# Kernel optimization log

Hardware: AMD Instinct MI355X
Metric: run time of the kernel (lower is better)

The kernel has to match this reference:

```python
import jax, jax.numpy as jnp
import numpy as np
from jax import lax

EPS = 1e-5
IC = 32  # inter_channels

def bn(x, g, b, m, v):
    sh = (1, -1, 1, 1)
    return (x - m.reshape(sh)) * (g.reshape(sh) * lax.rsqrt(v.reshape(sh) + EPS)) + b.reshape(sh)

def prelu(x, a):
    return jnp.where(x >= 0, x, a * x)

def conv1x1(x, w):  # x: [B,C,H,W], w: [O,C]
    return jnp.einsum('bchw,oc->bohw', x, w)

def dconv(x, w, d):  # 3x3 dilated conv, same padding
    return lax.conv_general_dilated(x, w, (1, 1), [(d, d), (d, d)], rhs_dilation=(d, d),
                                    dimension_numbers=('NCHW', 'OIHW', 'NCHW'))

def glca_forward(feature, q_w, q_gamma, q_beta, q_mean, q_var, q_alpha,
                 k_w, k_gamma, k_beta, k_mean, k_var, k_alpha,
                 v_w, v_gamma, v_beta, v_mean, v_var, v_alpha,
                 d1_w, d1_gamma, d1_beta, d1_mean, d1_var,
                 d2_w, d2_gamma, d2_beta, d2_mean, d2_var,
                 d3_w, d3_gamma, d3_beta, d3_mean, d3_var,
                 o_w, o_gamma, o_beta, o_mean, o_var, o_alpha):
    B, C, H, W = feature.shape
    q = prelu(bn(conv1x1(feature, q_w), q_gamma, q_beta, q_mean, q_var), q_alpha)  # [B,IC,H,W]
    k = prelu(bn(conv1x1(feature, k_w), k_gamma, k_beta, k_mean, k_var), k_alpha)
    val = prelu(bn(conv1x1(feature, v_w), v_gamma, v_beta, v_mean, v_var), v_alpha)
    qr = q.transpose(0, 3, 2, 1).reshape(B * W, H, IC)   # [BW,H,IC]
    kr = k.transpose(0, 3, 1, 2).reshape(B * W, IC, H)   # [BW,IC,H]
    att = jax.nn.softmax(jnp.matmul(qr, kr), axis=-1)    # [BW,H,H]
    branches = []
    for w, g, b, m, var, d in ((d1_w, d1_gamma, d1_beta, d1_mean, d1_var, 1),
                               (d2_w, d2_gamma, d2_beta, d2_mean, d2_var, 3),
                               (d3_w, d3_gamma, d3_beta, d3_mean, d3_var, 5)):
        t = jax.nn.relu(bn(dconv(val, w, d), g, b, m, var))          # [B,IC,H,W]
        # faithful to source: permute(0,3,1,2) then raw view to [BW,H,IC]
        t = t.transpose(0, 3, 1, 2).reshape(B * W, H, IC)
        branches.append(jnp.matmul(att, t))                          # [BW,H,IC]
    # faithful to source: cat along dim 0, then raw view(B,W,H,-1)
    res = jnp.concatenate(branches, axis=0).reshape(B, W, H, 3 * IC)
    res = res.transpose(0, 3, 2, 1)                                  # [B,3*IC,H,W]
    out = prelu(bn(conv1x1(res, o_w), o_gamma, o_beta, o_mean, o_var) + feature, o_alpha)
    return out

def setup_inputs() -> dict:
    B, C, H, W = 8, 256, 160, 160
    key = jax.random.key(0)
    ks = iter(jax.random.split(key, 48))
    d = {}
    d['feature'] = jax.random.normal(next(ks), (B, C, H, W), jnp.float32)
    for p in ('q', 'k', 'v'):
        d[p + '_w'] = jax.random.normal(next(ks), (IC, C), jnp.float32) * 0.05
        d[p + '_gamma'] = jax.random.uniform(next(ks), (IC,), jnp.float32, 0.5, 1.5)
        d[p + '_beta'] = jax.random.normal(next(ks), (IC,), jnp.float32) * 0.1
        d[p + '_mean'] = jax.random.normal(next(ks), (IC,), jnp.float32) * 0.1
        d[p + '_var'] = jax.random.uniform(next(ks), (IC,), jnp.float32, 0.5, 1.5)
        d[p + '_alpha'] = jnp.full((1,), 0.25, jnp.float32)
    for p in ('d1', 'd2', 'd3'):
        d[p + '_w'] = jax.random.normal(next(ks), (IC, IC, 3, 3), jnp.float32) * 0.05
        d[p + '_gamma'] = jax.random.uniform(next(ks), (IC,), jnp.float32, 0.5, 1.5)
        d[p + '_beta'] = jax.random.normal(next(ks), (IC,), jnp.float32) * 0.1
        d[p + '_mean'] = jax.random.normal(next(ks), (IC,), jnp.float32) * 0.1
        d[p + '_var'] = jax.random.uniform(next(ks), (IC,), jnp.float32, 0.5, 1.5)
    d['o_w'] = jax.random.normal(next(ks), (C, 3 * IC), jnp.float32) * 0.05
    d['o_gamma'] = jax.random.uniform(next(ks), (C,), jnp.float32, 0.5, 1.5)
    d['o_beta'] = jax.random.normal(next(ks), (C,), jnp.float32) * 0.1
    d['o_mean'] = jax.random.normal(next(ks), (C,), jnp.float32) * 0.1
    d['o_var'] = jax.random.uniform(next(ks), (C,), jnp.float32, 0.5, 1.5)
    d['o_alpha'] = jnp.full((1,), 0.25, jnp.float32)
    return d

def reference(feature, q_w, q_gamma, q_beta, q_mean, q_var, q_alpha,
              k_w, k_gamma, k_beta, k_mean, k_var, k_alpha,
              v_w, v_gamma, v_beta, v_mean, v_var, v_alpha,
              d1_w, d1_gamma, d1_beta, d1_mean, d1_var,
              d2_w, d2_gamma, d2_beta, d2_mean, d2_var,
              d3_w, d3_gamma, d3_beta, d3_mean, d3_var,
              o_w, o_gamma, o_beta, o_mean, o_var, o_alpha):
    return glca_forward(feature, q_w, q_gamma, q_beta, q_mean, q_var, q_alpha,
                        k_w, k_gamma, k_beta, k_mean, k_var, k_alpha,
                        v_w, v_gamma, v_beta, v_mean, v_var, v_alpha,
                        d1_w, d1_gamma, d1_beta, d1_mean, d1_var,
                        d2_w, d2_gamma, d2_beta, d2_mean, d2_var,
                        d3_w, d3_gamma, d3_beta, d3_mean, d3_var,
                        o_w, o_gamma, o_beta, o_mean, o_var, o_alpha)
```

## Files before the change

kernel.cpp:

```cpp
#include <hip/hip_runtime.h>

constexpr int Hh = 160, Ww = 160, Bb = 8, Cc = 256, ICn = 32;
constexpr int HWn = Hh * Ww;
constexpr float EPSf = 1e-5f;

constexpr int P_WQH  = 0;
constexpr int P_WQL  = 12288;
constexpr int P_QKVB = 24576;
constexpr int P_QKVA = 24672;
constexpr int P_DWB  = 24768;
constexpr int P_DB   = 52416;
constexpr int P_OWB  = 52512;
constexpr int P_OB   = 77088;
constexpr int P_OA   = 77344;
constexpr int PLANE  = Bb * ICn * HWn;
constexpr int OFF_Q  = 77824;
constexpr int OFF_K  = OFF_Q + PLANE;
constexpr int OFF_V  = OFF_Q + 2 * PLANE;
constexpr int OFF_T  = OFF_Q + 3 * PLANE;
constexpr int OFF_TPF= OFF_T + (3 * PLANE) / 2;
constexpr int OFF_CAT= OFF_Q + 6 * PLANE;

typedef unsigned short u16;
typedef short bf16x8 __attribute__((ext_vector_type(8)));
typedef float f32x4  __attribute__((ext_vector_type(4)));

__device__ __forceinline__ unsigned f2b(float x) {
    unsigned u = __float_as_uint(x);
    return (u + 0x7FFFu + ((u >> 16) & 1u)) >> 16;
}
__device__ __forceinline__ float b2f(unsigned b) { return __uint_as_float(b << 16); }

struct InPtrs { const float* p[40]; };

__global__ void k_prep(InPtrs in, float* __restrict__ ws) {
    int idx = blockIdx.x * 256 + threadIdx.x;
    if (idx < 24576) {
        int oc = idx >> 8, c = idx & 255;
        int z = oc >> 5, o = oc & 31;
        const float* wz = in.p[1 + 6 * z];
        float s = in.p[2 + 6 * z][o] * rsqrtf(in.p[5 + 6 * z][o] + EPSf);
        float wf = wz[o * 256 + c] * s;
        unsigned hi = f2b(wf);
        unsigned lo = f2b(wf - b2f(hi));
        ((u16*)(ws + P_WQH))[oc * 256 + c] = (u16)hi;
        ((u16*)(ws + P_WQL))[oc * 256 + c] = (u16)lo;
    } else if (idx < 24672) {
        int oc = idx - 24576; int z = oc >> 5, o = oc & 31;
        float s = in.p[2 + 6 * z][o] * rsqrtf(in.p[5 + 6 * z][o] + EPSf);
        ws[P_QKVB + oc] = in.p[3 + 6 * z][o] - in.p[4 + 6 * z][o] * s;
    } else if (idx < 24768) {
        int oc = idx - 24672; int z = oc >> 5;
        ws[P_QKVA + oc] = in.p[6 + 6 * z][0];
    } else if (idx < 52416) {
        int j = idx - 24768;
        int d = j / 9216, r2 = j % 9216;
        int oc = r2 & 31; int tmp = r2 >> 5;
        int kx = tmp % 3; tmp /= 3; int ky = tmp % 3; int ic2 = tmp / 3;
        const float* wd = in.p[19 + 5 * d];
        float s = in.p[20 + 5 * d][oc] * rsqrtf(in.p[23 + 5 * d][oc] + EPSf);
        float wf = wd[((oc * 32 + ic2) * 3 + ky) * 3 + kx] * s;
        ((u16*)(ws + P_DWB))[((d * 9 + ky * 3 + kx) * 32 + oc) * 32 + ic2] = (u16)f2b(wf);
    } else if (idx < 52512) {
        int j = idx - 52416; int d = j >> 5, oc = j & 31;
        float s = in.p[20 + 5 * d][oc] * rsqrtf(in.p[23 + 5 * d][oc] + EPSf);
        ws[P_DB + j] = in.p[21 + 5 * d][oc] - in.p[22 + 5 * d][oc] * s;
    } else if (idx < 77088) {
        int j2 = idx - 52512; int c = j2 / 96;
        float s = in.p[35][c] * rsqrtf(in.p[38][c] + EPSf);
        ((u16*)(ws + P_OWB))[j2] = (u16)f2b(in.p[34][j2] * s);
    } else if (idx < 77344) {
        int c = idx - 77088;
        float s = in.p[35][c] * rsqrtf(in.p[38][c] + EPSf);
        ws[P_OB + c] = in.p[36][c] - in.p[37][c] * s;
    } else if (idx == 77344) {
        ws[P_OA] = in.p[39][0];
    }
}

__global__ __launch_bounds__(64) void k_vpad(float* __restrict__ ws) {
    u16* Vt = (u16*)(ws + OFF_V);
    size_t base = (size_t)blockIdx.x * 176 * 32;
    int t = threadIdx.x;
    int off = (t < 32) ? t * 8 : (168 * 32 + (t - 32) * 8);
    uint4 z = {0u, 0u, 0u, 0u};
    *(uint4*)(Vt + base + off) = z;
}

__global__ __launch_bounds__(256) void k_qkv(const float* __restrict__ feat,
                                             float* __restrict__ ws) {
    __shared__ u16 BhS[8192];
    __shared__ u16 BlS[8192];
    const int tid = threadIdx.x;
    const int wv = tid >> 6, l = tid & 63;
    const int g = l >> 4, c15 = l & 15;
    const int n0 = blockIdx.x * 128;
    const int b = n0 / HWn, hw0 = n0 % HWn;
    const float* fbase = feat + (size_t)b * Cc * HWn + hw0;
    const u16* __restrict__ WQH = (const u16*)(ws + P_WQH);
    const u16* __restrict__ WQL = (const u16*)(ws + P_WQL);
    f32x4 acc[6][2];
    f32x4 z4 = {0.f, 0.f, 0.f, 0.f};
#pragma unroll
    for (int mt = 0; mt < 6; mt++) { acc[mt][0] = z4; acc[mt][1] = z4; }

    for (int kc = 0; kc < 4; kc++) {
        __syncthreads();
#pragma unroll
        for (int ss = 0; ss < 4; ss++) {
            int s = tid + ss * 256;
            int sl = s & 63, si = s >> 6;
            int k0 = kc * 64 + (si >> 3) * 32 + (sl >> 4) * 8;
            int nn = (si & 7) * 16 + (sl & 15);
            const float* gp = fbase + (size_t)k0 * HWn + nn;
            unsigned hb[8], lb[8];
#pragma unroll
            for (int v = 0; v < 8; v++) {
                float x = gp[(size_t)v * HWn];
                hb[v] = f2b(x);
                lb[v] = f2b(x - b2f(hb[v]));
            }
            uint4 hv = {hb[0] | (hb[1] << 16), hb[2] | (hb[3] << 16),
                        hb[4] | (hb[5] << 16), hb[6] | (hb[7] << 16)};
            uint4 lv = {lb[0] | (lb[1] << 16), lb[2] | (lb[3] << 16),
                        lb[4] | (lb[5] << 16), lb[6] | (lb[7] << 16)};
            *(uint4*)(&BhS[(si * 64 + sl) * 8]) = hv;
            *(uint4*)(&BlS[(si * 64 + sl) * 8]) = lv;
        }
        __syncthreads();
#pragma unroll
        for (int ks = 0; ks < 2; ks++) {
            bf16x8 bh[2], bl[2];
#pragma unroll
            for (int ntl = 0; ntl < 2; ntl++) {
                int nt = wv * 2 + ntl;
                bh[ntl] = *(const bf16x8*)(&BhS[((ks * 8 + nt) * 64 + l) * 8]);
                bl[ntl] = *(const bf16x8*)(&BlS[((ks * 8 + nt) * 64 + l) * 8]);
            }
#pragma unroll
            for (int mt = 0; mt < 6; mt++) {
                int arow = (16 * mt + c15) * 256 + kc * 64 + ks * 32 + g * 8;
                bf16x8 ah = *(const bf16x8*)(WQH + arow);
                bf16x8 al = *(const bf16x8*)(WQL + arow);
#pragma unroll
                for (int ntl = 0; ntl < 2; ntl++) {
                    acc[mt][ntl] = __builtin_amdgcn_mfma_f32_16x16x32_bf16(ah, bh[ntl], acc[mt][ntl], 0, 0, 0);
                    acc[mt][ntl] = __builtin_amdgcn_mfma_f32_16x16x32_bf16(ah, bl[ntl], acc[mt][ntl], 0, 0, 0);
                    acc[mt][ntl] = __builtin_amdgcn_mfma_f32_16x16x32_bf16(al, bh[ntl], acc[mt][ntl], 0, 0, 0);
                }
            }
        }
    }
    u16* vt = (u16*)(ws + OFF_V);
#pragma unroll
    for (int mt = 0; mt < 6; mt++)
#pragma unroll
        for (int ntl = 0; ntl < 2; ntl++) {
            int pos = hw0 + (wv * 2 + ntl) * 16 + c15;
            if (mt < 4) {
#pragma unroll
                for (int jr = 0; jr < 4; jr++) {
                    int oc = 16 * mt + 4 * g + jr;
                    float bb = ws[P_QKVB + oc];
                    float aa = ws[P_QKVA + oc];
                    float y = acc[mt][ntl][jr] + bb;
                    y = y >= 0.f ? y : aa * y;
                    int z = oc >> 5, o = oc & 31;
                    ws[OFF_Q + (size_t)z * PLANE + ((size_t)b * ICn + o) * HWn + pos] = y;
                }
            } else {
                int h = pos / 160, w2 = pos % 160;
                unsigned r[2];
#pragma unroll
                for (int p = 0; p < 2; p++) {
                    int oc = 16 * mt + 4 * g + 2 * p;
                    float y0 = acc[mt][ntl][2 * p]     + ws[P_QKVB + oc];
                    float y1 = acc[mt][ntl][2 * p + 1] + ws[P_QKVB + oc + 1];
                    float a0 = ws[P_QKVA + oc], a1 = ws[P_QKVA + oc + 1];
                    y0 = y0 >= 0.f ? y0 : a0 * y0;
                    y1 = y1 >= 0.f ? y1 : a1 * y1;
                    r[p] = f2b(y0) | (f2b(y1) << 16);
                }
                size_t a = ((size_t)(b * 160 + h) * 176 + w2 + 8) * 32 + (mt - 4) * 16 + 4 * g;
                uint2 dd; dd.x = r[0]; dd.y = r[1];
                *(uint2*)(vt + a) = dd;
            }
        }
}

__global__ __launch_bounds__(256) void k_dconv(float* __restrict__ ws) {
    const int tid = threadIdx.x;
    const int wv = tid >> 6, l = tid & 63;
    const int g = l >> 4, c15 = l & 15;
    const int b = blockIdx.y;
    const int d = blockIdx.z;
    const int dil = 1 + 2 * d;
    const int h0 = blockIdx.x * 2;
    const u16* __restrict__ WB = (const u16*)(ws + P_DWB) + d * 9 * 32 * 32;
    bf16x8 wb[9][2];
#pragma unroll
    for (int tap = 0; tap < 9; tap++)
#pragma unroll
        for (int n = 0; n < 2; n++)
            wb[tap][n] = *(const bf16x8*)(WB + ((size_t)tap * 32 + n * 16 + c15) * 32 + g * 8);
    const u16* __restrict__ Vt = (const u16*)(ws + OFF_V) + (size_t)b * 160 * 176 * 32;
    const float bias0 = ws[P_DB + d * 32 + c15];
    const float bias1 = ws[P_DB + d * 32 + 16 + c15];
    u16* __restrict__ tp = (u16*)(ws + OFF_TPF) + (size_t)(d * Bb + b) * ICn * HWn;
    f32x4 z4 = {0.f, 0.f, 0.f, 0.f};

    for (int t5 = 0; t5 < 5; t5++) {
        int t = wv * 5 + t5;
        int h = h0 + (t >= 10);
        int w0 = (t % 10) * 16;
        f32x4 acc0 = z4, acc1 = z4;
#pragma unroll
        for (int ky = 0; ky < 3; ky++) {
            int hh = h + dil * (ky - 1);
            if ((unsigned)hh >= 160u) continue;
            const u16* row = Vt + (size_t)hh * 176 * 32;
#pragma unroll
            for (int kx = 0; kx < 3; kx++) {
                int wbase = w0 + dil * (kx - 1) + 8;
                bf16x8 av = *(const bf16x8*)(row + (size_t)(wbase + c15) * 32 + g * 8);
                acc0 = __builtin_amdgcn_mfma_f32_16x16x32_bf16(av, wb[ky * 3 + kx][0], acc0, 0, 0, 0);
                acc1 = __builtin_amdgcn_mfma_f32_16x16x32_bf16(av, wb[ky * 3 + kx][1], acc1, 0, 0, 0);
            }
        }
        size_t pixb = (size_t)h * 160 + w0 + 4 * g;
        uint2 o0, o1;
        o0.x = f2b(fmaxf(acc0[0] + bias0, 0.f)) | (f2b(fmaxf(acc0[1] + bias0, 0.f)) << 16);
        o0.y = f2b(fmaxf(acc0[2] + bias0, 0.f)) | (f2b(fmaxf(acc0[3] + bias0, 0.f)) << 16);
        o1.x = f2b(fmaxf(acc1[0] + bias1, 0.f)) | (f2b(fmaxf(acc1[1] + bias1, 0.f)) << 16);
        o1.y = f2b(fmaxf(acc1[2] + bias1, 0.f)) | (f2b(fmaxf(acc1[3] + bias1, 0.f)) << 16);
        *(uint2*)(tp + (size_t)c15 * HWn + pixb) = o0;
        *(uint2*)(tp + (size_t)(16 + c15) * HWn + pixb) = o1;
    }
}

__global__ __launch_bounds__(256) void k_tfrag(float* __restrict__ ws) {
    __shared__ u16 fr[4][5120];
    const int tid = threadIdx.x;
    const int wq = blockIdx.x;
    const int b  = blockIdx.y;
    const int d  = blockIdx.z;
    const int w0 = wq * 4;
    const u16* __restrict__ tp = (const u16*)(ws + OFF_TPF) + (size_t)(d * Bb + b) * ICn * HWn;
    for (int i = tid; i < 5120; i += 256) {
        int ic = i / 160, h = i % 160;
        uint2 v = *(const uint2*)(tp + (size_t)ic * HWn + h * Ww + w0);
        fr[0][i] = (u16)(v.x & 0xFFFFu);
        fr[1][i] = (u16)(v.x >> 16);
        fr[2][i] = (u16)(v.y & 0xFFFFu);
        fr[3][i] = (u16)(v.y >> 16);
    }
    __syncthreads();
    u16* __restrict__ tf = (u16*)(ws + OFF_T);
#pragma unroll
    for (int it = 0; it < 10; it++) {
        int W = tid + it * 256;
        int s = W / 640, word = W % 640;
        int slot = word >> 6, lane = word & 63;
        int jc = (lane & 15) | ((slot / 5) << 4);
        int h2b = ((slot % 5) << 5) | (((lane >> 4) & 3) << 3);
        unsigned r[4];
#pragma unroll
        for (int p = 0; p < 4; p++) {
            int f0 = (h2b + 2 * p) * 32 + jc;
            unsigned lo = fr[s][f0];
            unsigned hi = fr[s][f0 + 32];
            r[p] = lo | (hi << 16);
        }
        uint4 o4 = {r[0], r[1], r[2], r[3]};
        *(uint4*)(tf + ((size_t)d * 1280 + b * 160 + w0 + s) * 5120 + word * 8) = o4;
    }
}

__device__ __forceinline__ void stage_qk_hilo(const float* __restrict__ g,
                                              char* hi_buf, char* lo_buf, int tid) {
#pragma unroll
    for (int ss = 0; ss < 2; ss++) {
        int s = tid + ss * 320;
        int l = s & 63, rt = s >> 6;
        int h = 16 * rt + (l & 15);
        int icb = (l >> 4) * 8;
        const float* gp = g + (size_t)icb * HWn + h * Ww;
        unsigned hb[8], lb[8];
#pragma unroll
        for (int v = 0; v < 8; v++) {
            float x = gp[(size_t)v * HWn];
            hb[v] = f2b(x);
            lb[v] = f2b(x - b2f(hb[v]));
        }
        uint4 hv = {hb[0] | (hb[1] << 16), hb[2] | (hb[3] << 16),
                    hb[4] | (hb[5] << 16), hb[6] | (hb[7] << 16)};
        uint4 lv = {lb[0] | (lb[1] << 16), lb[2] | (lb[3] << 16),
                    lb[4] | (lb[5] << 16), lb[6] | (lb[7] << 16)};
        *(uint4*)(hi_buf + s * 16) = hv;
        *(uint4*)(lo_buf + s * 16) = lv;
    }
}

__global__ __launch_bounds__(320) void k_att(float* __restrict__ ws) {
    extern __shared__ char smem[];
    char* q_hi = smem;
    char* q_lo = smem + 10240;
    char* k_hi = smem + 20480;
    char* k_lo = smem + 30720;
    char* Sb   = smem;
    const int tid = threadIdx.x;
    const int bid = blockIdx.x;
    const int r8 = bid & 7, qq = bid >> 3;
    const int b = qq / 20;
    const int w = r8 * 20 + (qq % 20);
    const int bw = b * Ww + w;
    const int wv = tid >> 6;
    const int l  = tid & 63;
    const int g  = l >> 4;
    const int c  = l & 15;

    const float* qg = ws + OFF_Q + (size_t)b * ICn * HWn + w;
    const float* kg = ws + OFF_K + (size_t)b * ICn * HWn + w;
    stage_qk_hilo(qg, q_hi, q_lo, tid);
    stage_qk_hilo(kg, k_hi, k_lo, tid);
    __syncthreads();

    bf16x8 bq[2][2];
#pragma unroll
    for (int ct = 0; ct < 2; ct++) {
        int tau = 2 * wv + ct;
        bq[ct][0] = *(bf16x8*)(q_hi + (tau * 64 + l) * 16);
        bq[ct][1] = *(bf16x8*)(q_lo + (tau * 64 + l) * 16);
    }
    f32x4 acc[10][2];
    f32x4 z4 = {0.f, 0.f, 0.f, 0.f};
#pragma unroll
    for (int rt = 0; rt < 10; rt++) { acc[rt][0] = z4; acc[rt][1] = z4; }
#pragma unroll
    for (int rt = 0; rt < 10; rt++) {
        bf16x8 ah = *(bf16x8*)(k_hi + (rt * 64 + l) * 16);
        bf16x8 al = *(bf16x8*)(k_lo + (rt * 64 + l) * 16);
#pragma unroll
        for (int ct = 0; ct < 2; ct++) {
            acc[rt][ct] = __builtin_amdgcn_mfma_f32_16x16x32_bf16(ah, bq[ct][0], acc[rt][ct], 0, 0, 0);
            acc[rt][ct] = __builtin_amdgcn_mfma_f32_16x16x32_bf16(ah, bq[ct][1], acc[rt][ct], 0, 0, 0);
            acc[rt][ct] = __builtin_amdgcn_mfma_f32_16x16x32_bf16(al, bq[ct][0], acc[rt][ct], 0, 0, 0);
        }
    }
    __syncthreads();

    float mx[2] = {-3.4e38f, -3.4e38f};
#pragma unroll
    for (int rt = 0; rt < 10; rt++)
#pragma unroll
        for (int ct = 0; ct < 2; ct++)
#pragma unroll
            for (int j = 0; j < 4; j++) mx[ct] = fmaxf(mx[ct], acc[rt][ct][j]);
#pragma unroll
    for (int ct = 0; ct < 2; ct++) {
        mx[ct] = fmaxf(mx[ct], __shfl_xor(mx[ct], 16));
        mx[ct] = fmaxf(mx[ct], __shfl_xor(mx[ct], 32));
    }
    float sm[2] = {0.f, 0.f};
#pragma unroll
    for (int rt = 0; rt < 10; rt++)
#pragma unroll
        for (int ct = 0; ct < 2; ct++)
#pragma unroll
            for (int j = 0; j < 4; j++) {
                float e = __expf(acc[rt][ct][j] - mx[ct]);
                acc[rt][ct][j] = e;
                sm[ct] += e;
            }
#pragma unroll
    for (int ct = 0; ct < 2; ct++) {
        sm[ct] += __shfl_xor(sm[ct], 16);
        sm[ct] += __shfl_xor(sm[ct], 32);
    }
    float inv[2] = {1.f / sm[0], 1.f / sm[1]};

#pragma unroll
    for (int rt = 0; rt < 10; rt++) {
#pragma unroll
        for (int ct = 0; ct < 2; ct++) {
            float p0 = acc[rt][ct][0] * inv[ct];
            float p1 = acc[rt][ct][1] * inv[ct];
            float p2 = acc[rt][ct][2] * inv[ct];
            float p3 = acc[rt][ct][3] * inv[ct];
            unsigned d0 = f2b(p0) | (f2b(p1) << 16);
            unsigned d1 = f2b(p2) | (f2b(p3) << 16);
            int Lf = c + 16 * (2 * (rt & 1) + (g >> 1));
            char* dst = Sb + (((wv * 2 + ct) * 5 + (rt >> 1)) * 64 + Lf) * 16 + 8 * (g & 1);
            uint2 dd; dd.x = d0; dd.y = d1;
            *(uint2*)dst = dd;
        }
    }
    __syncthreads();

    const u16* tf = (const u16*)(ws + OFF_T);
    u16* catb = (u16*)(ws + OFF_CAT);
    for (int d = 0; d < 3; d++) {
        const u16* tfd = tf + ((size_t)d * (Bb * Ww) + bw) * 5120;
        f32x4 po[2][2];
        po[0][0] = z4; po[0][1] = z4; po[1][0] = z4; po[1][1] = z4;
#pragma unroll
        for (int ks = 0; ks < 5; ks++) {
            bf16x8 a0 = *(const bf16x8*)(tfd + ((0 * 5 + ks) * 64 + l) * 8);
            bf16x8 a1 = *(const bf16x8*)(tfd + ((1 * 5 + ks) * 64 + l) * 8);
            bf16x8 s0 = *(bf16x8*)(Sb + (((wv * 2 + 0) * 5 + ks) * 64 + l) * 16);
            bf16x8 s1 = *(bf16x8*)(Sb + (((wv * 2 + 1) * 5 + ks) * 64 + l) * 16);
            po[0][0] = __builtin_amdgcn_mfma_f32_16x16x32_bf16(a0, s0, po[0][0], 0, 0, 0);
            po[0][1] = __builtin_amdgcn_mfma_f32_16x16x32_bf16(a0, s1, po[0][1], 0, 0, 0);
            po[1][0] = __builtin_amdgcn_mfma_f32_16x16x32_bf16(a1, s0, po[1][0], 0, 0, 0);
            po[1][1] = __builtin_amdgcn_mfma_f32_16x16x32_bf16(a1, s1, po[1][1], 0, 0, 0);
        }
#pragma unroll
        for (int jt = 0; jt < 2; jt++)
#pragma unroll
            for (int ct = 0; ct < 2; ct++) {
                int h1 = 32 * wv + 16 * ct + c;
                size_t idx = (size_t)d * PLANE + (size_t)bw * 5120 + h1 * 32 + 16 * jt + 4 * g;
                f32x4 v = po[jt][ct];
                uint2 dd;
                dd.x = f2b(v[0]) | (f2b(v[1]) << 16);
                dd.y = f2b(v[2]) | (f2b(v[3]) << 16);
                *(uint2*)(catb + idx) = dd;
            }
    }
}

__global__ __launch_bounds__(256) void k_out(const float* __restrict__ feat,
                                             const float* __restrict__ ws,
                                             float* __restrict__ out) {
    __shared__ u16 Bs[12288];
    const int tid = threadIdx.x;
    const int wv = tid >> 6, l = tid & 63;
    const int g = l >> 4, c15 = l & 15;
    const int n0 = blockIdx.x * 128;
    const int b = n0 / HWn, hw0 = n0 % HWn;
    const u16* __restrict__ CATb = (const u16*)(ws + OFF_CAT);
    const u16* __restrict__ OWB = (const u16*)(ws + P_OWB);

#pragma unroll
    for (int ss = 0; ss < 6; ss++) {
        int s = tid + ss * 256;
        int sl = s & 63, si = s >> 6;
        int p = (si & 7) * 16 + (sl & 15);
        int hw = hw0 + p;
        int h = hw / Ww, w2 = hw % Ww;
        int j = (si >> 3) * 32 + (sl >> 4) * 8;
        size_t flat = ((size_t)(b * Ww + w2) * Hh + h) * 96 + j;
        *(uint4*)(&Bs[(si * 64 + sl) * 8]) = *(const uint4*)(CATb + flat);
    }
    bf16x8 af[4][3];
#pragma unroll
    for (int mt = 0; mt < 4; mt++)
#pragma unroll
        for (int ks = 0; ks < 3; ks++)
            af[mt][ks] = *(const bf16x8*)(OWB + (wv * 64 + mt * 16 + c15) * 96 + ks * 32 + g * 8);
    __syncthreads();
    const float alpha = ws[P_OA];

    f32x4 z4 = {0.f, 0.f, 0.f, 0.f};
#pragma unroll
    for (int np = 0; np < 2; np++) {
        f32x4 acc[4][4];
#pragma unroll
        for (int mt = 0; mt < 4; mt++)
#pragma unroll
            for (int ntl = 0; ntl < 4; ntl++) acc[mt][ntl] = z4;
#pragma unroll
        for (int ks = 0; ks < 3; ks++) {
            bf16x8 bf_[4];
#pragma unroll
            for (int ntl = 0; ntl < 4; ntl++)
                bf_[ntl] = *(const bf16x8*)(&Bs[((ks * 8 + np * 4 + ntl) * 64 + l) * 8]);
#pragma unroll
            for (int mt = 0; mt < 4; mt++)
#pragma unroll
                for (int ntl = 0; ntl < 4; ntl++)
                    acc[mt][ntl] = __builtin_amdgcn_mfma_f32_16x16x32_bf16(af[mt][ks], bf_[ntl], acc[mt][ntl], 0, 0, 0);
        }
#pragma unroll
        for (int mt = 0; mt < 4; mt++)
#pragma unroll
            for (int ntl = 0; ntl < 4; ntl++) {
                int p = (np * 4 + ntl) * 16 + c15;
#pragma unroll
                for (int jr = 0; jr < 4; jr++) {
                    int cch = wv * 64 + mt * 16 + 4 * g + jr;
                    size_t base = ((size_t)b * Cc + cch) * HWn + hw0 + p;
                    float y = acc[mt][ntl][jr] + ws[P_OB + cch] + feat[base];
                    out[base] = y >= 0.f ? y : alpha * y;
                }
            }
    }
}

extern "C" void kernel_launch(void* const* d_in, const int* in_sizes, int n_in,
                              void* d_out, int out_size, void* d_ws, size_t ws_size,
                              hipStream_t stream) {
    InPtrs ip;
    for (int i = 0; i < 40; i++) ip.p[i] = (const float*)d_in[i];
    float* ws = (float*)d_ws;
    const float* feat = (const float*)d_in[0];
    float* out = (float*)d_out;

    k_prep<<<304, 256, 0, stream>>>(ip, ws);
    k_vpad<<<1280, 64, 0, stream>>>(ws);
    k_qkv<<<1600, 256, 0, stream>>>(feat, ws);
    k_dconv<<<dim3(80, 8, 3), 256, 0, stream>>>(ws);
    k_tfrag<<<dim3(40, 8, 3), 256, 0, stream>>>(ws);
    (void)hipFuncSetAttribute(reinterpret_cast<const void*>(k_att),
                              hipFuncAttributeMaxDynamicSharedMemorySize, 51200);
    k_att<<<1280, 320, 51200, stream>>>(ws);
    k_out<<<1600, 256, 0, stream>>>(feat, ws, out);
}
```

Before: 468.7 us.

## Double-buffer qkv feature tiles with direct global-to-LDS loads and wider blocks

Restructures the 1x1 qkv GEMM kernel so each block handles 256 pixels instead of 128. Raw fp32 feature tiles are loaded straight into LDS with global_load_lds, double-buffered across 8 k-chunks of 32 channels. The bf16 hi/lo split now happens when fragments are read from LDS, not when tiles are staged. The aim is to overlap global loads with MFMA work and to reuse each weight fragment across more columns. The cost is 64KB of dynamic LDS per block, which limits occupancy, and more accumulator registers.

Result: no change. 459.5 us (-2.0%).

```diff
diff --git a/kernel.cpp b/kernel.cpp
--- a/kernel.cpp
+++ b/kernel.cpp
@@ -30,6 +30,10 @@
     return (u + 0x7FFFu + ((u >> 16) & 1u)) >> 16;
 }
 __device__ __forceinline__ float b2f(unsigned b) { return __uint_as_float(b << 16); }
+
+#define GLOAD_LDS16(gp, lp) __builtin_amdgcn_global_load_lds( \
+    (const __attribute__((address_space(1))) void*)(gp), \
+    (__attribute__((address_space(3))) void*)(lp), 16, 0, 0)
 
 struct InPtrs { const float* p[40]; };
 
@@ -89,81 +93,87 @@
 
 __global__ __launch_bounds__(256) void k_qkv(const float* __restrict__ feat,
                                              float* __restrict__ ws) {
-    __shared__ u16 BhS[8192];
-    __shared__ u16 BlS[8192];
+    extern __shared__ float FS[];
     const int tid = threadIdx.x;
     const int wv = tid >> 6, l = tid & 63;
     const int g = l >> 4, c15 = l & 15;
-    const int n0 = blockIdx.x * 128;
+    const int n0 = blockIdx.x * 256;
     const int b = n0 / HWn, hw0 = n0 % HWn;
     const float* fbase = feat + (size_t)b * Cc * HWn + hw0;
     const u16* __restrict__ WQH = (const u16*)(ws + P_WQH);
     const u16* __restrict__ WQL = (const u16*)(ws + P_WQL);
-    f32x4 acc[6][2];
+
+    f32x4 acc[6][4];
     f32x4 z4 = {0.f, 0.f, 0.f, 0.f};
 #pragma unroll
-    for (int mt = 0; mt < 6; mt++) { acc[mt][0] = z4; acc[mt][1] = z4; }
-
-    for (int kc = 0; kc < 4; kc++) {
+    for (int mt = 0; mt < 6; mt++)
+#pragma unroll
+        for (int i = 0; i < 4; i++) acc[mt][i] = z4;
+
+#pragma unroll
+    for (int j = 0; j < 8; j++) {
+        int r = wv * 8 + j;
+        GLOAD_LDS16(fbase + (size_t)r * HWn + l * 4, &FS[r * 256]);
+    }
+    __syncthreads();
+
+    for (int kc = 0; kc < 8; kc++) {
+        if (kc < 7) {
+            float* dst = &FS[((kc + 1) & 1) * 8192];
+#pragma unroll
+            for (int j = 0; j < 8; j++) {
+                int r = wv * 8 + j;
+                GLOAD_LDS16(fbase + (size_t)((kc + 1) * 32 + r) * HWn + l * 4, dst + r * 256);
+            }
+        }
+        const float* B = &FS[(kc & 1) * 8192];
+        bf16x8 bh[4], bl[4];
+#pragma unroll
+        for (int i = 0; i < 4; i++) {
+            const float* bp = B + (g * 8) * 256 + (wv * 4 + i) * 16 + c15;
+            unsigned hw_[4], lw_[4];
+#pragma unroll
+            for (int v2 = 0; v2 < 4; v2++) {
+                float x0 = bp[(2 * v2) * 256];
+                float x1 = bp[(2 * v2 + 1) * 256];
+                unsigned h0 = f2b(x0), h1 = f2b(x1);
+                unsigned l0 = f2b(x0 - b2f(h0)), l1 = f2b(x1 - b2f(h1));
+                hw_[v2] = h0 | (h1 << 16);
+                lw_[v2] = l0 | (l1 << 16);
+            }
+            uint4 hv = {hw_[0], hw_[1], hw_[2], hw_[3]};
+            uint4 lv = {lw_[0], lw_[1], lw_[2], lw_[3]};
+            bh[i] = *(bf16x8*)&hv;
+            bl[i] = *(bf16x8*)&lv;
+        }
+#pragma unroll
+        for (int mt = 0; mt < 6; mt++) {
+            int arow = (16 * mt + c15) * 256 + kc * 32 + g * 8;
+            bf16x8 ah = *(const bf16x8*)(WQH + arow);
+            bf16x8 al = *(const bf16x8*)(WQL + arow);
+#pragma unroll
+            for (int i = 0; i < 4; i++) {
+                acc[mt][i] = __builtin_amdgcn_mfma_f32_16x16x32_bf16(ah, bh[i], acc[mt][i], 0, 0, 0);
+                acc[mt][i] = __builtin_amdgcn_mfma_f32_16x16x32_bf16(ah, bl[i], acc[mt][i], 0, 0, 0);
+                acc[mt][i] = __builtin_amdgcn_mfma_f32_16x16x32_bf16(al, bh[i], acc[mt][i], 0, 0, 0);
+            }
+        }
         __syncthreads();
-#pragma unroll
-        for (int ss = 0; ss < 4; ss++) {
-            int s = tid + ss * 256;
-            int sl = s & 63, si = s >> 6;
-            int k0 = kc * 64 + (si >> 3) * 32 + (sl >> 4) * 8;
-            int nn = (si & 7) * 16 + (sl & 15);
-            const float* gp = fbase + (size_t)k0 * HWn + nn;
-            unsigned hb[8], lb[8];
-#pragma unroll
-            for (int v = 0; v < 8; v++) {
-                float x = gp[(size_t)v * HWn];
-                hb[v] = f2b(x);
-                lb[v] = f2b(x - b2f(hb[v]));
-            }
-            uint4 hv = {hb[0] | (hb[1] << 16), hb[2] | (hb[3] << 16),
-                        hb[4] | (hb[5] << 16), hb[6] | (hb[7] << 16)};
-            uint4 lv = {lb[0] | (lb[1] << 16), lb[2] | (lb[3] << 16),
-                        lb[4] | (lb[5] << 16), lb[6] | (lb[7] << 16)};
-            *(uint4*)(&BhS[(si * 64 + sl) * 8]) = hv;
-            *(uint4*)(&BlS[(si * 64 + sl) * 8]) = lv;
-        }
-        __syncthreads();
-#pragma unroll
-        for (int ks = 0; ks < 2; ks++) {
-            bf16x8 bh[2], bl[2];
-#pragma unroll
-            for (int ntl = 0; ntl < 2; ntl++) {
-                int nt = wv * 2 + ntl;
-                bh[ntl] = *(const bf16x8*)(&BhS[((ks * 8 + nt) * 64 + l) * 8]);
-                bl[ntl] = *(const bf16x8*)(&BlS[((ks * 8 + nt) * 64 + l) * 8]);
-            }
-#pragma unroll
-            for (int mt = 0; mt < 6; mt++) {
-                int arow = (16 * mt + c15) * 256 + kc * 64 + ks * 32 + g * 8;
-                bf16x8 ah = *(const bf16x8*)(WQH + arow);
-                bf16x8 al = *(const bf16x8*)(WQL + arow);
-#pragma unroll
-                for (int ntl = 0; ntl < 2; ntl++) {
-                    acc[mt][ntl] = __builtin_amdgcn_mfma_f32_16x16x32_bf16(ah, bh[ntl], acc[mt][ntl], 0, 0, 0);
-                    acc[mt][ntl] = __builtin_amdgcn_mfma_f32_16x16x32_bf16(ah, bl[ntl], acc[mt][ntl], 0, 0, 0);
-                    acc[mt][ntl] = __builtin_amdgcn_mfma_f32_16x16x32_bf16(al, bh[ntl], acc[mt][ntl], 0, 0, 0);
-                }
-            }
-        }
-    }
+    }
+
     u16* vt = (u16*)(ws + OFF_V);
 #pragma unroll
     for (int mt = 0; mt < 6; mt++)
 #pragma unroll
-        for (int ntl = 0; ntl < 2; ntl++) {
-            int pos = hw0 + (wv * 2 + ntl) * 16 + c15;
+        for (int i = 0; i < 4; i++) {
+            int pos = hw0 + (wv * 4 + i) * 16 + c15;
             if (mt < 4) {
 #pragma unroll
                 for (int jr = 0; jr < 4; jr++) {
                     int oc = 16 * mt + 4 * g + jr;
                     float bb = ws[P_QKVB + oc];
                     float aa = ws[P_QKVA + oc];
-                    float y = acc[mt][ntl][jr] + bb;
+                    float y = acc[mt][i][jr] + bb;
                     y = y >= 0.f ? y : aa * y;
                     int z = oc >> 5, o = oc & 31;
                     ws[OFF_Q + (size_t)z * PLANE + ((size_t)b * ICn + o) * HWn + pos] = y;
@@ -174,8 +184,8 @@
 #pragma unroll
                 for (int p = 0; p < 2; p++) {
                     int oc = 16 * mt + 4 * g + 2 * p;
-                    float y0 = acc[mt][ntl][2 * p]     + ws[P_QKVB + oc];
-                    float y1 = acc[mt][ntl][2 * p + 1] + ws[P_QKVB + oc + 1];
+                    float y0 = acc[mt][i][2 * p]     + ws[P_QKVB + oc];
+                    float y1 = acc[mt][i][2 * p + 1] + ws[P_QKVB + oc + 1];
                     float a0 = ws[P_QKVA + oc], a1 = ws[P_QKVA + oc + 1];
                     y0 = y0 >= 0.f ? y0 : a0 * y0;
                     y1 = y1 >= 0.f ? y1 : a1 * y1;
@@ -508,7 +518,9 @@
 
     k_prep<<<304, 256, 0, stream>>>(ip, ws);
     k_vpad<<<1280, 64, 0, stream>>>(ws);
-    k_qkv<<<1600, 256, 0, stream>>>(feat, ws);
+    (void)hipFuncSetAttribute(reinterpret_cast<const void*>(k_qkv),
+                              hipFuncAttributeMaxDynamicSharedMemorySize, 65536);
+    k_qkv<<<800, 256, 65536, stream>>>(feat, ws);
     k_dconv<<<dim3(80, 8, 3), 256, 0, stream>>>(ws);
     k_tfrag<<<dim3(40, 8, 3), 256, 0, stream>>>(ws);
     (void)hipFuncSetAttribute(reinterpret_cast<const void*>(k_att),
```
